# Performance work log

Hardware: AMD Instinct MI355X
Metric: run time of the kernel (lower is better)

The kernel has to match this reference:

```python
import jax, jax.numpy as jnp
import numpy as np

EMB = 1024
HEADS = 16
HEAD_DIM = EMB // HEADS
EPS = 1e-5


def setup_inputs() -> dict:
    key = jax.random.key(0)
    ks = jax.random.split(key, 10)
    B, T, D = 2, 2048, EMB
    s = 1.0 / np.sqrt(D)
    inp = {
        "x": jax.random.normal(ks[0], (B, T, D), dtype=jnp.float32),
        "wq": jax.random.normal(ks[1], (D, D), dtype=jnp.float32) * s,
        "bq": jnp.zeros((D,), jnp.float32),
        "wk": jax.random.normal(ks[2], (D, D), dtype=jnp.float32) * s,
        "bk": jnp.zeros((D,), jnp.float32),
        "wv": jax.random.normal(ks[3], (D, D), dtype=jnp.float32) * s,
        "bv": jnp.zeros((D,), jnp.float32),
        "wo": jax.random.normal(ks[4], (D, D), dtype=jnp.float32) * s,
        "bo": jnp.zeros((D,), jnp.float32),
        "gamma": jnp.ones((D,), jnp.float32),
        "beta": jnp.zeros((D,), jnp.float32),
    }
    return inp


def _attention(x, wq, bq, wk, bk, wv, bv, wo, bo, gamma, beta):
    B, T, D = x.shape
    H, Hd = HEADS, HEAD_DIM
    q = (x @ wq + bq).reshape(B, T, H, Hd)
    k = (x @ wk + bk).reshape(B, T, H, Hd)
    v = (x @ wv + bv).reshape(B, T, H, Hd)
    # scores: [B, H, T, T]
    scores = jnp.einsum("bthd,bshd->bhts", q, k) / np.sqrt(Hd)
    attn = jax.nn.softmax(scores, axis=-1)  # dropout is identity in eval
    ctx = jnp.einsum("bhts,bshd->bthd", attn, v).reshape(B, T, D)
    out = ctx @ wo + bo
    y = x + out  # residual (dropout identity)
    mu = jnp.mean(y, axis=-1, keepdims=True)
    var = jnp.var(y, axis=-1, keepdims=True)
    return (y - mu) * jax.lax.rsqrt(var + EPS) * gamma + beta


def reference(x, wq, bq, wk, bk, wv, bv, wo, bo, gamma, beta):
    return _attention(x, wq, bq, wk, bk, wv, bv, wo, bo, gamma, beta)
```

## Files before the change

kernel.cpp:

```cpp
#include <hip/hip_runtime.h>

#define BSZ   2
#define TSEQ  2048
#define DMOD  1024
#define NHEAD 16
#define HDIM  64
#define MROW  (BSZ*TSEQ)
#define LNEPS 1e-5f
#define QSCALE 0.18033688011f

typedef __bf16 bf16x8 __attribute__((ext_vector_type(8)));
typedef float  f32x4  __attribute__((ext_vector_type(4)));
typedef unsigned short us8 __attribute__((ext_vector_type(8)));
typedef unsigned short us4 __attribute__((ext_vector_type(4)));

__device__ __forceinline__ unsigned short f2bf(float f) {
    unsigned u = __float_as_uint(f);
    u += 0x7FFF + ((u >> 16) & 1);
    return (unsigned short)(u >> 16);
}
__device__ __forceinline__ float bf2f(unsigned short u) {
    return __uint_as_float((unsigned)u << 16);
}

__device__ __forceinline__ float fexp2(float x) {
#if __has_builtin(__builtin_amdgcn_exp2f)
    return __builtin_amdgcn_exp2f(x);
#else
    return __expf(x * 0.6931471805599453f);
#endif
}

__device__ __forceinline__ void gld_lds16(const void* g, void* l) {
    __builtin_amdgcn_global_load_lds(
        (const __attribute__((address_space(1))) unsigned int*)g,
        (__attribute__((address_space(3))) unsigned int*)l, 16, 0, 0);
}

__global__ __launch_bounds__(256) void prep_k(
    const float* __restrict__ x,
    const float* __restrict__ wq, const float* __restrict__ wk,
    const float* __restrict__ wv, const float* __restrict__ wo,
    unsigned short* __restrict__ Xb,
    unsigned short* __restrict__ WqkvT, unsigned short* __restrict__ WoT)
{
    const int tid = threadIdx.x;
    if (blockIdx.x < 2048) {
        const size_t i = ((size_t)blockIdx.x * 256 + tid) * 8;
        float4 a = *(const float4*)&x[i];
        float4 b = *(const float4*)&x[i + 4];
        union { unsigned short u[8]; uint4 v; } o;
        o.u[0]=f2bf(a.x); o.u[1]=f2bf(a.y); o.u[2]=f2bf(a.z); o.u[3]=f2bf(a.w);
        o.u[4]=f2bf(b.x); o.u[5]=f2bf(b.y); o.u[6]=f2bf(b.z); o.u[7]=f2bf(b.w);
        *(uint4*)&Xb[i] = o.v;
        return;
    }
    __shared__ float T[64][68];
    const int id = blockIdx.x - 2048;
    const int z  = id >> 8;
    const int bx = id & 15;
    const int by = (id >> 4) & 15;
    const float* W = (z == 0) ? wq : (z == 1) ? wk : (z == 2) ? wv : wo;
    unsigned short* Wt = (z < 3) ? (WqkvT + (size_t)z*1024*1024) : WoT;
    const int lr = tid >> 4, lc = (tid & 15) * 4;
    #pragma unroll
    for (int p = 0; p < 4; ++p) {
        const int kk = p*16 + lr;
        float4 v = *(const float4*)&W[(size_t)(by*64 + kk)*1024 + bx*64 + lc];
        T[lc+0][kk] = v.x; T[lc+1][kk] = v.y; T[lc+2][kk] = v.z; T[lc+3][kk] = v.w;
    }
    __syncthreads();
    #pragma unroll
    for (int p = 0; p < 2; ++p) {
        const int nl = p*32 + (tid >> 3);
        const int kb = (tid & 7) * 8;
        float4 a = *(const float4*)&T[nl][kb];
        float4 b = *(const float4*)&T[nl][kb+4];
        union { unsigned short u[8]; uint4 v; } o;
        o.u[0]=f2bf(a.x); o.u[1]=f2bf(a.y); o.u[2]=f2bf(a.z); o.u[3]=f2bf(a.w);
        o.u[4]=f2bf(b.x); o.u[5]=f2bf(b.y); o.u[6]=f2bf(b.z); o.u[7]=f2bf(b.w);
        *(uint4*)&Wt[(size_t)(bx*64 + nl)*1024 + by*64 + kb] = o.v;
    }
}

struct GemmFrags {
    const unsigned short* Ag[4]; const unsigned short* Bg[4];
    unsigned short *la[4], *lb[4];
    const unsigned short *ap[4][2], *bp[4][2];
};

__device__ __forceinline__ void gemm_setup(
    GemmFrags& F, unsigned short* As, unsigned short* Bs,
    const unsigned short* A, const unsigned short* Bt,
    int bm, int bn, int lda)
{
    const int tid  = threadIdx.x;
    const int wv   = tid >> 6;
    const int lane = tid & 63;
    const int quad = lane >> 4;
    const int l16  = lane & 15;
    const int wm   = wv & 1, wn = wv >> 1;
    const int r_l = lane >> 3;
    const int c_l = lane & 7;
    #pragma unroll
    for (int s = 0; s < 4; ++s) {
        const int i = wv*4 + s;
        const int R = i*8 + r_l;
        const int gc = (c_l ^ (R & 7)) * 8;
        F.Ag[s] = A  + (size_t)(bm + R)*lda + gc;
        F.Bg[s] = Bt + (size_t)(bn + R)*lda + gc;
        F.la[s] = As + i*512;
        F.lb[s] = Bs + i*512;
    }
    #pragma unroll
    for (int t = 0; t < 4; ++t)
        #pragma unroll
        for (int kh = 0; kh < 2; ++kh) {
            const int ra = wm*64 + t*16 + l16;
            const int rb = wn*64 + t*16 + l16;
            F.ap[t][kh] = &As[ra*64 + ((kh*4 + quad) ^ (ra & 7))*8];
            F.bp[t][kh] = &Bs[rb*64 + ((kh*4 + quad) ^ (rb & 7))*8];
        }
}

__device__ __forceinline__ void gemm_kloop(
    GemmFrags& F, f32x4 (&acc)[4][4], int k_begin, int k_end)
{
    for (int k0 = k_begin; k0 < k_end; k0 += 64) {
        __syncthreads();
        #pragma unroll
        for (int s = 0; s < 4; ++s) {
            gld_lds16(F.Ag[s] + k0, F.la[s]);
            gld_lds16(F.Bg[s] + k0, F.lb[s]);
        }
        __syncthreads();
        #pragma unroll
        for (int kh = 0; kh < 2; ++kh) {
            bf16x8 af[4], bfr[4];
            #pragma unroll
            for (int t = 0; t < 4; ++t) {
                af[t]  = *(const bf16x8*)F.ap[t][kh];
                bfr[t] = *(const bf16x8*)F.bp[t][kh];
            }
            #pragma unroll
            for (int i = 0; i < 4; ++i)
                #pragma unroll
                for (int j = 0; j < 4; ++j)
                    acc[i][j] = __builtin_amdgcn_mfma_f32_16x16x32_bf16(af[i], bfr[j], acc[i][j], 0, 0, 0);
        }
    }
}

__global__ __launch_bounds__(256) void gemm_qkv_k(
    const unsigned short* __restrict__ A, const unsigned short* __restrict__ Bt,
    const float* __restrict__ b0, const float* __restrict__ b1,
    const float* __restrict__ b2,
    unsigned short* __restrict__ oQ, unsigned short* __restrict__ oK,
    unsigned short* __restrict__ oV)
{
    __shared__ unsigned short As[128*64];
    __shared__ unsigned short Bs[128*64];
    const int tid  = threadIdx.x;
    const int wv   = tid >> 6;
    const int lane = tid & 63;
    const int quad = lane >> 4;
    const int l16  = lane & 15;
    const int wm   = wv & 1, wn = wv >> 1;
    const int bm = blockIdx.y * 128, bn = blockIdx.x * 128;

    GemmFrags F;
    gemm_setup(F, As, Bs, A, Bt, bm, bn, 1024);

    f32x4 acc[4][4];
    #pragma unroll
    for (int i = 0; i < 4; ++i)
        #pragma unroll
        for (int j = 0; j < 4; ++j) acc[i][j] = (f32x4){0.f,0.f,0.f,0.f};

    gemm_kloop(F, acc, 0, 1024);

    const int seg = bn >> 10;
    const float* bias = (seg == 0) ? b0 : (seg == 1) ? b1 : b2;
    const int cb = bn & 1023;
    if (seg < 2) {
        unsigned short* O = (seg == 0) ? oQ : oK;
        const float sc = (seg == 0) ? QSCALE : 1.0f;
        #pragma unroll
        for (int nt = 0; nt < 4; ++nt) {
            const int col = cb + wn*64 + nt*16 + l16;
            const float bs = bias[col];
            #pragma unroll
            for (int mt = 0; mt < 4; ++mt)
                #pragma unroll
                for (int r = 0; r < 4; ++r) {
                    const int grow = bm + wm*64 + mt*16 + quad*4 + r;
                    O[(size_t)grow*1024 + col] = f2bf((acc[mt][nt][r] + bs) * sc);
                }
        }
    } else {
        #pragma unroll
        for (int nt = 0; nt < 4; ++nt) {
            const int ch = cb + wn*64 + nt*16 + l16;
            const float bs = bias[ch];
            #pragma unroll
            for (int mt = 0; mt < 4; ++mt) {
                const int grow0 = bm + wm*64 + mt*16 + quad*4;
                us4 o;
                #pragma unroll
                for (int r = 0; r < 4; ++r) o[r] = f2bf(acc[mt][nt][r] + bs);
                *(us4*)&oV[(size_t)ch*MROW + grow0] = o;
            }
        }
    }
}

__global__ __launch_bounds__(256) void gemm_proj_k(
    const unsigned short* __restrict__ A, const unsigned short* __restrict__ Bt,
    unsigned short* __restrict__ P)
{
    __shared__ unsigned short As[128*64];
    __shared__ unsigned short Bs[128*64];
    const int tid  = threadIdx.x;
    const int wv   = tid >> 6;
    const int lane = tid & 63;
    const int quad = lane >> 4;
    const int l16  = lane & 15;
    const int wm   = wv & 1, wn = wv >> 1;
    const int bm = blockIdx.y * 128, bn = blockIdx.x * 128;
    const int kz = blockIdx.z;

    GemmFrags F;
    gemm_setup(F, As, Bs, A, Bt, bm, bn, 1024);

    f32x4 acc[4][4];
    #pragma unroll
    for (int i = 0; i < 4; ++i)
        #pragma unroll
        for (int j = 0; j < 4; ++j) acc[i][j] = (f32x4){0.f,0.f,0.f,0.f};

    gemm_kloop(F, acc, kz*512, kz*512 + 512);

    unsigned short* O = P + (size_t)kz*MROW*1024;
    #pragma unroll
    for (int nt = 0; nt < 4; ++nt) {
        const int col = bn + wn*64 + nt*16 + l16;
        #pragma unroll
        for (int mt = 0; mt < 4; ++mt)
            #pragma unroll
            for (int r = 0; r < 4; ++r) {
                const int grow = bm + wm*64 + mt*16 + quad*4 + r;
                O[(size_t)grow*1024 + col] = f2bf(acc[mt][nt][r]);
            }
    }
}

__global__ __launch_bounds__(256, 2) void attn_k(
    const unsigned short* __restrict__ Qg,
    const unsigned short* __restrict__ Kg,
    const unsigned short* __restrict__ Vtg,
    unsigned short* __restrict__ CTX)
{
    __shared__ __align__(16) char lds_raw[51200];
    unsigned short* Qs = (unsigned short*)lds_raw;
    unsigned short* Ks = (unsigned short*)(lds_raw + 18432);
    unsigned short* Vs = (unsigned short*)(lds_raw + 34816);
    float* Od = (float*)lds_raw;
    float* Ld = (float*)(lds_raw + 34816);

    const int tid  = threadIdx.x;
    const int wv   = tid >> 6;
    const int lane = tid & 63;
    const int quad = lane >> 4;
    const int l16  = lane & 15;
    const int wq   = wv & 1;
    const int wk   = wv >> 1;
    const int qb   = blockIdx.x * 128;
    const int h    = blockIdx.y;
    const int b    = blockIdx.z;

    {
        const int row = tid & 127, cb = (tid >> 7) * 32;
        const unsigned short* Qrow = Qg + ((size_t)(b*TSEQ + qb + row))*DMOD + h*HDIM + cb;
        #pragma unroll
        for (int j = 0; j < 4; ++j)
            *(us8*)&Qs[row*72 + cb + j*8] = *(const us8*)&Qrow[j*8];
    }
    __syncthreads();
    bf16x8 qf[4][2];
    #pragma unroll
    for (int nt = 0; nt < 4; ++nt)
        #pragma unroll
        for (int kh = 0; kh < 2; ++kh)
            qf[nt][kh] = *(const bf16x8*)&Qs[(wq*64 + nt*16 + l16)*72 + kh*32 + quad*8];

    const int sr = lane >> 3;
    const int sc = lane & 7;
    const bool isK = (wv < 2);
    const int half = wv & 1;
    const unsigned short* gbase;
    unsigned int goff[8];
    unsigned short* ldst;
    if (isK) {
        gbase = Kg + ((size_t)(b*TSEQ + half*1024))*DMOD + h*HDIM;
        #pragma unroll
        for (int s = 0; s < 8; ++s) {
            const int R = s*8 + sr;
            const int gc = sc ^ ((R ^ (R >> 2)) & 7);
            goff[s] = (unsigned)(R*DMOD + gc*8);
        }
        ldst = Ks + half*4096;
    } else {
        gbase = Vtg + ((size_t)(h*HDIM))*MROW + b*TSEQ + half*1024;
        #pragma unroll
        for (int s = 0; s < 8; ++s) {
            const int D = s*8 + sr;
            const int gc = sc ^ (D & 7);
            goff[s] = (unsigned)(D*MROW + gc*8);
        }
        ldst = Vs + half*4096;
    }
    const size_t gstep = isK ? (size_t)64*DMOD : (size_t)64;

    const int rowA_l = (l16 >> 2)*8 + (l16 & 3);
    const int rowB_l = rowA_l + 4;
    const int swA = (rowA_l ^ (rowA_l >> 2)) & 7;
    const int swB = (rowB_l ^ (rowB_l >> 2)) & 7;
    const unsigned short* KsW = Ks + wk*4096;
    const unsigned short* VsW = Vs + wk*4096;

    bf16x8 onef;
    { union { unsigned short u[8]; bf16x8 v; } o1;
      #pragma unroll
      for (int i = 0; i < 8; ++i) o1.u[i] = 0x3F80;
      onef = o1.v; }

    f32x4 oacc[4][4];
    f32x4 lacc[4];
    #pragma unroll
    for (int dt = 0; dt < 4; ++dt)
        #pragma unroll
        for (int nt = 0; nt < 4; ++nt) oacc[dt][nt] = (f32x4){0.f,0.f,0.f,0.f};
    #pragma unroll
    for (int nt = 0; nt < 4; ++nt) lacc[nt] = (f32x4){0.f,0.f,0.f,0.f};

    for (int it = 0; it < 16; ++it) {
        __syncthreads();
        #pragma unroll
        for (int s = 0; s < 8; ++s)
            gld_lds16(gbase + (size_t)it*gstep + goff[s], ldst + s*512);
        __syncthreads();

        #pragma unroll
        for (int gl = 0; gl < 2; ++gl) {
            const int rA = gl*32 + rowA_l;
            const int rB = gl*32 + rowB_l;
            bf16x8 ka0 = *(const bf16x8*)&KsW[rA*64 + ((quad     ^ swA))*8];
            bf16x8 ka1 = *(const bf16x8*)&KsW[rA*64 + (((4+quad) ^ swA))*8];
            bf16x8 kb0 = *(const bf16x8*)&KsW[rB*64 + ((quad     ^ swB))*8];
            bf16x8 kb1 = *(const bf16x8*)&KsW[rB*64 + (((4+quad) ^ swB))*8];
            bf16x8 vf[4];
            #pragma unroll
            for (int dt = 0; dt < 4; ++dt)
                vf[dt] = *(const bf16x8*)&VsW[(dt*16 + l16)*64 + ((gl*4 + quad) ^ (l16 & 7))*8];

            #pragma unroll
            for (int nt = 0; nt < 4; ++nt) {
                f32x4 z = (f32x4){0.f,0.f,0.f,0.f};
                z = __builtin_amdgcn_mfma_f32_16x16x32_bf16(ka0, qf[nt][0], z, 0, 0, 0);
                f32x4 sA = __builtin_amdgcn_mfma_f32_16x16x32_bf16(ka1, qf[nt][1], z, 0, 0, 0);
                z = (f32x4){0.f,0.f,0.f,0.f};
                z = __builtin_amdgcn_mfma_f32_16x16x32_bf16(kb0, qf[nt][0], z, 0, 0, 0);
                f32x4 sB = __builtin_amdgcn_mfma_f32_16x16x32_bf16(kb1, qf[nt][1], z, 0, 0, 0);

                float eA[4], eB[4];
                #pragma unroll
                for (int r = 0; r < 4; ++r) { eA[r] = fexp2(sA[r]); eB[r] = fexp2(sB[r]); }
                union { unsigned d[4]; bf16x8 v; } up;
                up.d[0] = __builtin_amdgcn_perm(__float_as_uint(eA[1]), __float_as_uint(eA[0]), 0x07060302);
                up.d[1] = __builtin_amdgcn_perm(__float_as_uint(eA[3]), __float_as_uint(eA[2]), 0x07060302);
                up.d[2] = __builtin_amdgcn_perm(__float_as_uint(eB[1]), __float_as_uint(eB[0]), 0x07060302);
                up.d[3] = __builtin_amdgcn_perm(__float_as_uint(eB[3]), __float_as_uint(eB[2]), 0x07060302);
                const bf16x8 pf = up.v;

                lacc[nt] = __builtin_amdgcn_mfma_f32_16x16x32_bf16(onef, pf, lacc[nt], 0, 0, 0);
                #pragma unroll
                for (int dt = 0; dt < 4; ++dt)
                    oacc[dt][nt] = __builtin_amdgcn_mfma_f32_16x16x32_bf16(vf[dt], pf, oacc[dt][nt], 0, 0, 0);
            }
        }
    }

    __syncthreads();
    if (wk == 0) {
        float* od = Od + wq*64*68;
        #pragma unroll
        for (int nt = 0; nt < 4; ++nt) {
            #pragma unroll
            for (int dt = 0; dt < 4; ++dt)
                *(f32x4*)&od[(nt*16 + l16)*68 + dt*16 + quad*4] = oacc[dt][nt];
            if (quad == 0) Ld[wq*64 + nt*16 + l16] = lacc[nt][0];
        }
    }
    __syncthreads();
    if (wk == 1) {
        const float* od = Od + wq*64*68;
        #pragma unroll
        for (int nt = 0; nt < 4; ++nt) {
            const float l = Ld[wq*64 + nt*16 + l16] + lacc[nt][0];
            const float inv = 1.f / l;
            const int q = qb + wq*64 + nt*16 + l16;
            unsigned short* crow = CTX + ((size_t)(b*TSEQ + q))*DMOD + h*HDIM;
            #pragma unroll
            for (int dt = 0; dt < 4; ++dt) {
                f32x4 p = *(const f32x4*)&od[(nt*16 + l16)*68 + dt*16 + quad*4];
                us4 o;
                #pragma unroll
                for (int r = 0; r < 4; ++r) o[r] = f2bf((p[r] + oacc[dt][nt][r]) * inv);
                *(us4*)&crow[dt*16 + quad*4] = o;
            }
        }
    }
}

__global__ __launch_bounds__(256) void red_ln_k(
    const float* __restrict__ x, const unsigned short* __restrict__ P,
    const float* __restrict__ bo,
    const float* __restrict__ gamma, const float* __restrict__ beta,
    float* __restrict__ out)
{
    __shared__ float rs[4], rss[4];
    const int row = blockIdx.x;
    const int tid = threadIdx.x;
    const int c = tid * 4;
    const float4 xv = *(const float4*)&x[(size_t)row*DMOD + c];
    const us4 p0 = *(const us4*)&P[(size_t)row*DMOD + c];
    const us4 p1 = *(const us4*)&P[(size_t)(MROW + row)*DMOD + c];
    const float4 bv4 = *(const float4*)&bo[c];
    const float v0 = xv.x + bf2f(p0[0]) + bf2f(p1[0]) + bv4.x;
    const float v1 = xv.y + bf2f(p0[1]) + bf2f(p1[1]) + bv4.y;
    const float v2 = xv.z + bf2f(p0[2]) + bf2f(p1[2]) + bv4.z;
    const float v3 = xv.w + bf2f(p0[3]) + bf2f(p1[3]) + bv4.w;
    float s  = v0 + v1 + v2 + v3;
    float ss = v0*v0 + v1*v1 + v2*v2 + v3*v3;
    #pragma unroll
    for (int o = 32; o > 0; o >>= 1) {
        s  += __shfl_down(s,  o, 64);
        ss += __shfl_down(ss, o, 64);
    }
    if ((tid & 63) == 0) { rs[tid >> 6] = s; rss[tid >> 6] = ss; }
    __syncthreads();
    s  = rs[0] + rs[1] + rs[2] + rs[3];
    ss = rss[0] + rss[1] + rss[2] + rss[3];
    const float mean = s * (1.f/DMOD);
    const float var  = ss * (1.f/DMOD) - mean*mean;
    const float rstd = rsqrtf(var + LNEPS);
    const float4 gv = *(const float4*)&gamma[c];
    const float4 bv = *(const float4*)&beta[c];
    float4 o;
    o.x = (v0 - mean)*rstd*gv.x + bv.x;
    o.y = (v1 - mean)*rstd*gv.y + bv.y;
    o.z = (v2 - mean)*rstd*gv.z + bv.z;
    o.w = (v3 - mean)*rstd*gv.w + bv.w;
    *(float4*)&out[(size_t)row*DMOD + c] = o;
}

extern "C" void kernel_launch(void* const* d_in, const int* in_sizes, int n_in,
                              void* d_out, int out_size, void* d_ws, size_t ws_size,
                              hipStream_t stream) {
    const float* x     = (const float*)d_in[0];
    const float* wq    = (const float*)d_in[1];
    const float* bq    = (const float*)d_in[2];
    const float* wk    = (const float*)d_in[3];
    const float* bk    = (const float*)d_in[4];
    const float* wvp   = (const float*)d_in[5];
    const float* bvp   = (const float*)d_in[6];
    const float* wo    = (const float*)d_in[7];
    const float* bo    = (const float*)d_in[8];
    const float* gamma = (const float*)d_in[9];
    const float* beta  = (const float*)d_in[10];
    float* out = (float*)d_out;

    unsigned short* Xb    = (unsigned short*)d_ws;
    unsigned short* WqkvT = Xb    + (size_t)MROW*DMOD;
    unsigned short* WoT   = WqkvT + (size_t)3072*1024;
    unsigned short* Qb    = WoT   + (size_t)1024*1024;
    unsigned short* Kb    = Qb    + (size_t)MROW*DMOD;
    unsigned short* VtG   = Kb    + (size_t)MROW*DMOD;
    unsigned short* CTXb  = VtG   + (size_t)DMOD*MROW;
    unsigned short* Pp    = Qb;

    prep_k<<<3072, 256, 0, stream>>>(x, wq, wk, wvp, wo, Xb, WqkvT, WoT);

    gemm_qkv_k<<<dim3(3072/128, MROW/128), 256, 0, stream>>>(
        Xb, WqkvT, bq, bk, bvp, Qb, Kb, VtG);

    attn_k<<<dim3(TSEQ/128, NHEAD, BSZ), 256, 0, stream>>>(Qb, Kb, VtG, CTXb);

    gemm_proj_k<<<dim3(DMOD/128, MROW/128, 2), 256, 0, stream>>>(CTXb, WoT, Pp);

    red_ln_k<<<MROW, 256, 0, stream>>>(x, Pp, bo, gamma, beta, out);
}
```

Before: 195.3 us.

## Load GEMM B fragments directly from global memory instead of staging through LDS

The B operand of both projection GEMMs is no longer copied into shared memory. Each wave now reads its own MFMA B fragments straight from global memory into registers. This halves LDS usage per block and removes B's LDS writes and reads, which could raise occupancy. In exchange, the two waves that share the same wn columns each fetch that B tile from global memory, and these loads are not coalesced the way the cooperative LDS fill was. The loads also sit between the barriers, so their latency is exposed.

Result: slower. 229.2 us (+17.4%).

```diff
diff --git a/kernel.cpp b/kernel.cpp
--- a/kernel.cpp
+++ b/kernel.cpp
@@ -84,13 +84,14 @@
 }
 
 struct GemmFrags {
-    const unsigned short* Ag[4]; const unsigned short* Bg[4];
-    unsigned short *la[4], *lb[4];
-    const unsigned short *ap[4][2], *bp[4][2];
+    const unsigned short* Ag[4];
+    unsigned short* la[4];
+    const unsigned short* ap[4][2];
+    const unsigned short* Bp[4];
 };
 
 __device__ __forceinline__ void gemm_setup(
-    GemmFrags& F, unsigned short* As, unsigned short* Bs,
+    GemmFrags& F, unsigned short* As,
     const unsigned short* A, const unsigned short* Bt,
     int bm, int bn, int lda)
 {
@@ -107,20 +108,18 @@
         const int i = wv*4 + s;
         const int R = i*8 + r_l;
         const int gc = (c_l ^ (R & 7)) * 8;
-        F.Ag[s] = A  + (size_t)(bm + R)*lda + gc;
-        F.Bg[s] = Bt + (size_t)(bn + R)*lda + gc;
+        F.Ag[s] = A + (size_t)(bm + R)*lda + gc;
         F.la[s] = As + i*512;
-        F.lb[s] = Bs + i*512;
-    }
-    #pragma unroll
-    for (int t = 0; t < 4; ++t)
+    }
+    #pragma unroll
+    for (int t = 0; t < 4; ++t) {
         #pragma unroll
         for (int kh = 0; kh < 2; ++kh) {
             const int ra = wm*64 + t*16 + l16;
-            const int rb = wn*64 + t*16 + l16;
             F.ap[t][kh] = &As[ra*64 + ((kh*4 + quad) ^ (ra & 7))*8];
-            F.bp[t][kh] = &Bs[rb*64 + ((kh*4 + quad) ^ (rb & 7))*8];
-        }
+        }
+        F.Bp[t] = Bt + (size_t)(bn + wn*64 + t*16 + l16)*lda + quad*8;
+    }
 }
 
 __device__ __forceinline__ void gemm_kloop(
@@ -129,24 +128,27 @@
     for (int k0 = k_begin; k0 < k_end; k0 += 64) {
         __syncthreads();
         #pragma unroll
-        for (int s = 0; s < 4; ++s) {
+        for (int s = 0; s < 4; ++s)
             gld_lds16(F.Ag[s] + k0, F.la[s]);
-            gld_lds16(F.Bg[s] + k0, F.lb[s]);
+        bf16x8 b0[4], b1[4];
+        #pragma unroll
+        for (int t = 0; t < 4; ++t) {
+            b0[t] = *(const bf16x8*)(F.Bp[t] + k0);
+            b1[t] = *(const bf16x8*)(F.Bp[t] + k0 + 32);
         }
         __syncthreads();
         #pragma unroll
         for (int kh = 0; kh < 2; ++kh) {
-            bf16x8 af[4], bfr[4];
-            #pragma unroll
-            for (int t = 0; t < 4; ++t) {
-                af[t]  = *(const bf16x8*)F.ap[t][kh];
-                bfr[t] = *(const bf16x8*)F.bp[t][kh];
-            }
+            bf16x8 af[4];
+            #pragma unroll
+            for (int t = 0; t < 4; ++t)
+                af[t] = *(const bf16x8*)F.ap[t][kh];
             #pragma unroll
             for (int i = 0; i < 4; ++i)
                 #pragma unroll
                 for (int j = 0; j < 4; ++j)
-                    acc[i][j] = __builtin_amdgcn_mfma_f32_16x16x32_bf16(af[i], bfr[j], acc[i][j], 0, 0, 0);
+                    acc[i][j] = __builtin_amdgcn_mfma_f32_16x16x32_bf16(
+                        af[i], kh ? b1[j] : b0[j], acc[i][j], 0, 0, 0);
         }
     }
 }
@@ -159,7 +161,6 @@
     unsigned short* __restrict__ oV)
 {
     __shared__ unsigned short As[128*64];
-    __shared__ unsigned short Bs[128*64];
     const int tid  = threadIdx.x;
     const int wv   = tid >> 6;
     const int lane = tid & 63;
@@ -169,7 +170,7 @@
     const int bm = blockIdx.y * 128, bn = blockIdx.x * 128;
 
     GemmFrags F;
-    gemm_setup(F, As, Bs, A, Bt, bm, bn, 1024);
+    gemm_setup(F, As, A, Bt, bm, bn, 1024);
 
     f32x4 acc[4][4];
     #pragma unroll
@@ -219,7 +220,6 @@
     unsigned short* __restrict__ P)
 {
     __shared__ unsigned short As[128*64];
-    __shared__ unsigned short Bs[128*64];
     const int tid  = threadIdx.x;
     const int wv   = tid >> 6;
     const int lane = tid & 63;
@@ -230,7 +230,7 @@
     const int kz = blockIdx.z;
 
     GemmFrags F;
-    gemm_setup(F, As, Bs, A, Bt, bm, bn, 1024);
+    gemm_setup(F, As, A, Bt, bm, bn, 1024);
 
     f32x4 acc[4][4];
     #pragma unroll
```
